# Optimization experiments

Hardware: AMD Instinct MI355X
Metric: run time of the kernel (lower is better)

Reference implementation:

```python
import jax, jax.numpy as jnp
import numpy as np

Q, N, S, A, E, H = 2048, 64, 128, 4, 128, 8
D = E // H
NEG = -1e9

def _mlp(x, w1, b1, w2, b2):
    return jax.nn.silu(x @ w1 + b1) @ w2 + b2

def _mha(x, wq, bq, wk, bk, wv, bv, wo, bo):
    # MultiHeadAttention with default activation=relu applied to q,k,v and output
    q = jax.nn.relu(x @ wq + bq)
    k = jax.nn.relu(x @ wk + bk)
    v = jax.nn.relu(x @ wv + bv)
    def split(t):
        return t.reshape(Q, N, H, D).transpose(0, 2, 1, 3)  # [Q,H,N,D]
    qh, kh, vh = split(q), split(k), split(v)
    scores = jnp.einsum('bhqd,bhkd->bhqk', qh, kh) / (D ** 0.5)
    attn = jax.nn.softmax(scores, axis=-1)
    y = jnp.einsum('bhqk,bhkd->bhqd', attn, vh).transpose(0, 2, 1, 3).reshape(Q, N, E)
    return jax.nn.relu(y @ wo + bo)

def setup_inputs():
    key = jax.random.key(0)
    ks = jax.random.split(key, 26)
    nrm = lambda k, s: jax.random.normal(k, s, jnp.float32) * 0.05
    return {
        'tasks': jax.random.normal(ks[0], (Q, N, N + 4 * S), jnp.float32),
        'constraints': jax.random.normal(ks[1], (Q, A), jnp.float32),
        'masks': jax.random.randint(ks[2], (Q, N, S), 0, 2),
        'topologicals': jax.random.randint(ks[3], (Q, N), 0, N),
        'w_init1': nrm(ks[4], (N + A, 128)), 'b_init1': jnp.zeros((128,), jnp.float32),
        'w_init2': nrm(ks[5], (128, E)), 'b_init2': jnp.zeros((E,), jnp.float32),
        'wq': nrm(ks[6], (E, E)), 'bq': jnp.zeros((E,), jnp.float32),
        'wk': nrm(ks[7], (E, E)), 'bk': jnp.zeros((E,), jnp.float32),
        'wv': nrm(ks[8], (E, E)), 'bv': jnp.zeros((E,), jnp.float32),
        'wo': nrm(ks[9], (E, E)), 'bo': jnp.zeros((E,), jnp.float32),
        'w_node1': nrm(ks[10], (E + A, 128)), 'b_node1': jnp.zeros((128,), jnp.float32),
        'w_node2': nrm(ks[11], (128, E)), 'b_node2': jnp.zeros((E,), jnp.float32),
        'w_ser1': nrm(ks[12], (A, 128)), 'b_ser1': jnp.zeros((128,), jnp.float32),
        'w_ser2': nrm(ks[13], (128, E)), 'b_ser2': jnp.zeros((E,), jnp.float32),
    }

def reference(tasks, constraints, masks, topologicals,
              w_init1, b_init1, w_init2, b_init2,
              wq, bq, wk, bk, wv, bv, wo, bo,
              w_node1, b_node1, w_node2, b_node2,
              w_ser1, b_ser1, w_ser2, b_ser2):
    cons = jnp.broadcast_to(constraints[:, None, :], (Q, N, A))
    node_emb = _mlp(jnp.concatenate([tasks[:, :, :N], cons], -1), w_init1, b_init1, w_init2, b_init2)
    nodes_emb = _mha(node_emb, wq, bq, wk, bk, wv, bv, wo, bo) + node_emb
    # original sets channel 0 to -3 then overwrites with 3; channel 2 stays 0 (kept faithfully)
    qos = jnp.zeros((Q, N, A), jnp.float32).at[:, :, 0].set(3.0).at[:, :, 1].set(1.0).at[:, :, 3].set(1.0)
    ava = jnp.ones((Q,), jnp.float32)
    tp = jnp.full((Q,), 3.0, jnp.float32)
    rel = jnp.ones((Q,), jnp.float32)
    ridx = jnp.zeros((Q, N), jnp.float32)
    rprob = jnp.zeros((Q, N), jnp.float32)
    qidx = jnp.arange(Q)
    topo_seq = topologicals[:, ::-1].T  # [N, Q]: reversed topological order, one node per step
    keys = jax.random.split(jax.random.key(1), N)

    def step(carry, xs):
        qos, ava, tp, rel, ridx, rprob = carry
        topo, k = xs
        task = tasks[qidx, topo]                 # [Q, N + 4S] per-query gathered row
        workflow = task[:, :N]
        response_time = jnp.max(workflow * qos[:, :, 0], axis=1)  # [Q]
        qos_feat = jnp.stack([response_time, ava, tp, rel], axis=-1)
        node_e = nodes_emb[qidx, topo]           # [Q, E]
        tne = _mlp(jnp.concatenate([node_e, qos_feat], -1), w_node1, b_node1, w_node2, b_node2)
        services = task[:, N:].reshape(Q, S, A)
        ser_emb = _mlp(services, w_ser1, b_ser1, w_ser2, b_ser2)
        logits = jnp.einsum('qse,qe->qs', ser_emb, tne)
        mask = masks[qidx, topo]                 # [Q, S]
        logits = jnp.where(mask == 0, NEG, logits)
        ser_prob = jax.nn.softmax(logits, axis=-1)
        ser_idx = jax.random.categorical(k, logits)  # ~ Categorical(ser_prob)
        onehot = jax.nn.one_hot(topo, N, dtype=jnp.float32)
        ridx = ridx + onehot * ser_idx[:, None].astype(jnp.float32)
        rprob = rprob + onehot * ser_prob[qidx, ser_idx][:, None]
        base = ser_idx * 4 + N
        ser_rt = task[qidx, base]
        ser_ava = task[qidx, base + 1]
        ser_tp = task[qidx, base + 2]
        ser_rel = task[qidx, base + 3]
        new_tp = jnp.minimum(ser_tp, tp)
        qos = qos.at[qidx, topo, 0].set(ser_rt + response_time)
        qos = qos.at[qidx, topo, 1].set(ser_ava * ava)
        qos = qos.at[qidx, topo, 2].set(new_tp)
        qos = qos.at[qidx, topo, 3].set(ser_rel * rel)
        return (qos, ser_ava * ava, new_tp, ser_rel * rel, ridx, rprob), None

    (qos, ava, tp, rel, ridx, rprob), _ = jax.lax.scan(
        step, (qos, ava, tp, rel, ridx, rprob), (topo_seq, keys))
    return ridx.astype(jnp.int16), rprob
```

## Files before the change

### kernel.cpp

```cpp
#include <hip/hip_runtime.h>
#include <math.h>

#define Qn 2048
#define Nn 64
#define Sn 128
#define An 4
#define En 128
#define TASKW 576
#define NEGV -1000000000.0f

typedef float v2f __attribute__((ext_vector_type(2)));

__device__ __forceinline__ v2f mkv2(float a, float b) {
  v2f r; r.x = a; r.y = b; return r;
}
__device__ __forceinline__ void pkfma(v2f& d, v2f a, v2f b) {
  asm("v_pk_fma_f32 %0, %1, %2, %0" : "+v"(d) : "v"(a), "v"(b));
}
__device__ __forceinline__ v2f pkmul(v2f a, v2f b) {
  v2f d; asm("v_pk_mul_f32 %0, %1, %2" : "=v"(d) : "v"(a), "v"(b)); return d;
}
__device__ __forceinline__ v2f pkadd(v2f a, v2f b) {
  v2f d; asm("v_pk_add_f32 %0, %1, %2" : "=v"(d) : "v"(a), "v"(b)); return d;
}

__device__ __forceinline__ void threefry2x32(unsigned k0, unsigned k1,
                                             unsigned x0, unsigned x1,
                                             unsigned& o0, unsigned& o1) {
  unsigned ks2 = k0 ^ k1 ^ 0x1BD11BDAu;
  x0 += k0; x1 += k1;
#define TFR(r) { x0 += x1; x1 = (x1 << (r)) | (x1 >> (32 - (r))); x1 ^= x0; }
  TFR(13) TFR(15) TFR(26) TFR(6)
  x0 += k1;  x1 += ks2 + 1u;
  TFR(17) TFR(29) TFR(16) TFR(24)
  x0 += ks2; x1 += k0 + 2u;
  TFR(13) TFR(15) TFR(26) TFR(6)
  x0 += k0;  x1 += k1 + 3u;
  TFR(17) TFR(29) TFR(16) TFR(24)
  x0 += k1;  x1 += ks2 + 4u;
  TFR(13) TFR(15) TFR(26) TFR(6)
  x0 += ks2; x1 += k0 + 5u;
#undef TFR
  o0 = x0; o1 = x1;
}

__device__ __forceinline__ float silu_f(float x) {
  return x / (1.0f + expf(-x));
}

__device__ __forceinline__ float fexp(float x) {
  return __builtin_amdgcn_exp2f(x * 1.44269504088896f);
}
__device__ __forceinline__ float fsilu(float x) {
  const float e = __builtin_amdgcn_exp2f(x * -1.44269504088896f);
  return x * __builtin_amdgcn_rcpf(1.0f + e);
}
__device__ __forceinline__ float flog(float x) {
  return __builtin_amdgcn_logf(x) * 0.69314718055995f;
}

__global__ void setup_kernel(const float* __restrict__ w_node2,
                             const float* __restrict__ b_node2,
                             const float* __restrict__ w_ser2,
                             const float* __restrict__ b_ser2,
                             float* __restrict__ Mbuf, float* __restrict__ dvec,
                             unsigned* __restrict__ keys) {
  const int b = blockIdx.x, t = threadIdx.x;
  if (b < 128) {
    float acc = 0.0f;
    for (int e = 0; e < 128; ++e)
      acc = fmaf(w_node2[b * 128 + e], w_ser2[t * 128 + e], acc);
    Mbuf[b * 128 + t] = acc;
  } else if (b == 128) {
    float acc = 0.0f;
    for (int e = 0; e < 128; ++e)
      acc = fmaf(b_node2[e], w_ser2[t * 128 + e], acc);
    dvec[t] = acc;
  } else {
    if (t < 64) {
      unsigned o0, o1;
      threefry2x32(0u, 1u, 0u, (unsigned)t, o0, o1);
      keys[2 * t + 0] = o0;
      keys[2 * t + 1] = o1;
    }
  }
}

__global__ __launch_bounds__(256, 2)
void init_mlp_kernel(const float* __restrict__ tasks,
                     const float* __restrict__ cons,
                     const float* __restrict__ w1, const float* __restrict__ b1,
                     const float* __restrict__ w2, const float* __restrict__ b2,
                     float* __restrict__ node_emb) {
  const int q = blockIdx.x, tid = threadIdx.x;
  const int lane = tid & 127, half = tid >> 7;
  __shared__ __align__(16) float xr[2][68];
  __shared__ __align__(16) float sgb[2][128];
  v2f w1p[34], w2p[64];
#pragma unroll
  for (int i = 0; i < 34; ++i)
    w1p[i] = mkv2(w1[(2 * i) * 128 + lane], w1[(2 * i + 1) * 128 + lane]);
#pragma unroll
  for (int j = 0; j < 64; ++j)
    w2p[j] = mkv2(w2[(2 * j) * 128 + lane], w2[(2 * j + 1) * 128 + lane]);
  const float bb1 = b1[lane], bb2 = b2[lane];
  for (int r = 0; r < 64; r += 2) {
    if (tid < 136) {
      const int rr = tid / 68, j = tid - rr * 68;
      xr[rr][j] = (j < 64) ? tasks[(q * 64 + r + rr) * TASKW + j]
                           : cons[q * 4 + (j - 64)];
    }
    __syncthreads();
    v2f gp = mkv2(0.0f, 0.0f);
    const v2f* xr2 = (const v2f*)&xr[half][0];
#pragma unroll
    for (int i = 0; i < 34; ++i) pkfma(gp, xr2[i], w1p[i]);
    const float g = gp.x + gp.y + bb1;
    sgb[half][lane] = silu_f(g);
    __syncthreads();
    v2f op = mkv2(0.0f, 0.0f);
    const v2f* sgb2 = (const v2f*)&sgb[half][0];
#pragma unroll
    for (int j = 0; j < 64; ++j) pkfma(op, sgb2[j], w2p[j]);
    node_emb[(q * 64 + r + half) * 128 + lane] = op.x + op.y + bb2;
    __syncthreads();
  }
}

__global__ __launch_bounds__(256, 2)
void mha_kernel(const float* __restrict__ node_emb,
                const float* __restrict__ wq, const float* __restrict__ bq,
                const float* __restrict__ wk, const float* __restrict__ bk,
                const float* __restrict__ wv, const float* __restrict__ bv,
                float* __restrict__ y_out) {
  const int q = blockIdx.x, tid = threadIdx.x;
  __shared__ __align__(16) float xs[64][130];
  __shared__ __align__(16) float qh[64][18];
  __shared__ __align__(16) float kh[64][18];
  __shared__ __align__(16) float vt[16][66];
  __shared__ __align__(16) float pool[3 * 16 * 130];
  float (*wht)[16][130] = (float (*)[16][130])pool;
  float (*at)[66] = (float (*)[66])pool;

  for (int idx = tid; idx < 64 * 128; idx += 256) {
    const int n = idx >> 7, e = idx & 127;
    xs[n][e] = node_emb[(q * 64 + n) * 128 + e];
  }
  __syncthreads();

  const int d16 = tid >> 4;
  const int ng = tid & 15;

  for (int hd = 0; hd < 8; ++hd) {
    for (int idx = tid; idx < 3 * 128 * 16; idx += 256) {
      const int m = idx >> 11, k = (idx >> 4) & 127, d = idx & 15;
      const float* W = (m == 0) ? wq : (m == 1) ? wk : wv;
      wht[m][d][k] = W[k * 128 + hd * 16 + d];
    }
    __syncthreads();

    {
      const float bqv = bq[hd * 16 + d16];
      const float bkv = bk[hd * 16 + d16];
      const float bvv = bv[hd * 16 + d16];
      const v2f* wq2 = (const v2f*)&wht[0][d16][0];
      const v2f* wk2 = (const v2f*)&wht[1][d16][0];
      const v2f* wv2 = (const v2f*)&wht[2][d16][0];
      const v2f* xr0 = (const v2f*)&xs[ng][0];
      const v2f* xr1 = (const v2f*)&xs[ng + 16][0];
      const v2f* xr2 = (const v2f*)&xs[ng + 32][0];
      const v2f* xr3 = (const v2f*)&xs[ng + 48][0];
      v2f aq0 = mkv2(0, 0), aq1 = mkv2(0, 0), aq2 = mkv2(0, 0), aq3 = mkv2(0, 0);
      v2f ak0 = mkv2(0, 0), ak1 = mkv2(0, 0), ak2 = mkv2(0, 0), ak3 = mkv2(0, 0);
      v2f av0 = mkv2(0, 0), av1 = mkv2(0, 0), av2 = mkv2(0, 0), av3 = mkv2(0, 0);
#pragma unroll 8
      for (int kk = 0; kk < 64; ++kk) {
        const v2f wqv = wq2[kk], wkv = wk2[kk], wvv = wv2[kk];
        const v2f x0 = xr0[kk], x1 = xr1[kk], x2 = xr2[kk], x3 = xr3[kk];
        pkfma(aq0, x0, wqv); pkfma(aq1, x1, wqv);
        pkfma(aq2, x2, wqv); pkfma(aq3, x3, wqv);
        pkfma(ak0, x0, wkv); pkfma(ak1, x1, wkv);
        pkfma(ak2, x2, wkv); pkfma(ak3, x3, wkv);
        pkfma(av0, x0, wvv); pkfma(av1, x1, wvv);
        pkfma(av2, x2, wvv); pkfma(av3, x3, wvv);
      }
      qh[ng][d16] = fmaxf(aq0.x + aq0.y + bqv, 0.0f);
      qh[ng + 16][d16] = fmaxf(aq1.x + aq1.y + bqv, 0.0f);
      qh[ng + 32][d16] = fmaxf(aq2.x + aq2.y + bqv, 0.0f);
      qh[ng + 48][d16] = fmaxf(aq3.x + aq3.y + bqv, 0.0f);
      kh[ng][d16] = fmaxf(ak0.x + ak0.y + bkv, 0.0f);
      kh[ng + 16][d16] = fmaxf(ak1.x + ak1.y + bkv, 0.0f);
      kh[ng + 32][d16] = fmaxf(ak2.x + ak2.y + bkv, 0.0f);
      kh[ng + 48][d16] = fmaxf(ak3.x + ak3.y + bkv, 0.0f);
      vt[d16][ng] = fmaxf(av0.x + av0.y + bvv, 0.0f);
      vt[d16][ng + 16] = fmaxf(av1.x + av1.y + bvv, 0.0f);
      vt[d16][ng + 32] = fmaxf(av2.x + av2.y + bvv, 0.0f);
      vt[d16][ng + 48] = fmaxf(av3.x + av3.y + bvv, 0.0f);
    }
    __syncthreads();

    {
      const int n = tid >> 2, mg = tid & 3;
      v2f qv[8];
      const v2f* qrow = (const v2f*)&qh[n][0];
#pragma unroll
      for (int kk = 0; kk < 8; ++kk) qv[kk] = qrow[kk];
#pragma unroll 4
      for (int jj = 0; jj < 16; ++jj) {
        const int m = mg + 4 * jj;
        const v2f* krow = (const v2f*)&kh[m][0];
        v2f accp = mkv2(0.0f, 0.0f);
#pragma unroll
        for (int kk = 0; kk < 8; ++kk) pkfma(accp, qv[kk], krow[kk]);
        at[n][m] = (accp.x + accp.y) * 0.25f;
      }
    }
    __syncthreads();

    {
      const int r = tid >> 2, p = tid & 3;
      float mx = -1e30f;
#pragma unroll
      for (int t2 = 0; t2 < 16; ++t2) mx = fmaxf(mx, at[r][p * 16 + t2]);
      mx = fmaxf(mx, __shfl_xor(mx, 1, 64));
      mx = fmaxf(mx, __shfl_xor(mx, 2, 64));
      float s = 0.0f;
#pragma unroll
      for (int t2 = 0; t2 < 16; ++t2) {
        const float e = fexp(at[r][p * 16 + t2] - mx);
        at[r][p * 16 + t2] = e;
        s += e;
      }
      s += __shfl_xor(s, 1, 64);
      s += __shfl_xor(s, 2, 64);
      const float rs = __builtin_amdgcn_rcpf(s);
#pragma unroll
      for (int t2 = 0; t2 < 16; ++t2) at[r][p * 16 + t2] *= rs;
    }
    __syncthreads();

    {
      const int dd = tid & 15, ngr = tid >> 4;
      const v2f* vrow = (const v2f*)&vt[dd][0];
      const v2f* ar0 = (const v2f*)&at[ngr][0];
      const v2f* ar1 = (const v2f*)&at[ngr + 16][0];
      const v2f* ar2 = (const v2f*)&at[ngr + 32][0];
      const v2f* ar3 = (const v2f*)&at[ngr + 48][0];
      v2f ac0 = mkv2(0, 0), ac1 = mkv2(0, 0), ac2 = mkv2(0, 0), ac3 = mkv2(0, 0);
#pragma unroll 8
      for (int kk = 0; kk < 32; ++kk) {
        const v2f vv = vrow[kk];
        pkfma(ac0, ar0[kk], vv);
        pkfma(ac1, ar1[kk], vv);
        pkfma(ac2, ar2[kk], vv);
        pkfma(ac3, ar3[kk], vv);
      }
      y_out[(q * 64 + ngr) * 128 + hd * 16 + dd] = ac0.x + ac0.y;
      y_out[(q * 64 + ngr + 16) * 128 + hd * 16 + dd] = ac1.x + ac1.y;
      y_out[(q * 64 + ngr + 32) * 128 + hd * 16 + dd] = ac2.x + ac2.y;
      y_out[(q * 64 + ngr + 48) * 128 + hd * 16 + dd] = ac3.x + ac3.y;
    }
    __syncthreads();
  }
}

__global__ __launch_bounds__(256, 4)
void outproj_kernel(const float* __restrict__ node_emb,
                    const float* __restrict__ wo, const float* __restrict__ bo,
                    float* __restrict__ nodes_emb) {
  const int q = blockIdx.x, tid = threadIdx.x;
  __shared__ __align__(16) float ys[64][130];
  __shared__ __align__(16) float wot[32][130];
  for (int idx = tid; idx < 64 * 128; idx += 256) {
    const int n = idx >> 7, e = idx & 127;
    ys[n][e] = nodes_emb[(q * 64 + n) * 128 + e];
  }
  const int cg = tid & 15, ngr = tid >> 4;
  for (int c0 = 0; c0 < 128; c0 += 32) {
    __syncthreads();
    for (int idx = tid; idx < 32 * 128; idx += 256) {
      const int k = idx >> 5, c = idx & 31;
      wot[c][k] = wo[k * 128 + c0 + c];
    }
    __syncthreads();
    const int c = c0 + 2 * cg;
    const v2f* w0 = (const v2f*)&wot[2 * cg][0];
    const v2f* w1 = (const v2f*)&wot[2 * cg + 1][0];
    const v2f* yr0 = (const v2f*)&ys[ngr][0];
    const v2f* yr1 = (const v2f*)&ys[ngr + 16][0];
    const v2f* yr2 = (const v2f*)&ys[ngr + 32][0];
    const v2f* yr3 = (const v2f*)&ys[ngr + 48][0];
    v2f a00 = mkv2(0, 0), a01 = mkv2(0, 0), a10 = mkv2(0, 0), a11 = mkv2(0, 0);
    v2f a20 = mkv2(0, 0), a21 = mkv2(0, 0), a30 = mkv2(0, 0), a31 = mkv2(0, 0);
#pragma unroll 8
    for (int kk = 0; kk < 64; ++kk) {
      const v2f wv0 = w0[kk], wv1 = w1[kk];
      const v2f x0 = yr0[kk], x1 = yr1[kk], x2 = yr2[kk], x3 = yr3[kk];
      pkfma(a00, x0, wv0); pkfma(a01, x0, wv1);
      pkfma(a10, x1, wv0); pkfma(a11, x1, wv1);
      pkfma(a20, x2, wv0); pkfma(a21, x2, wv1);
      pkfma(a30, x3, wv0); pkfma(a31, x3, wv1);
    }
    const float b0v = bo[c], b1v = bo[c + 1];
#define OUTP_EMIT(J, A0, A1)                                                  \
    {                                                                         \
      const int n = ngr + 16 * J;                                             \
      const float2 res = *(const float2*)&node_emb[(q * 64 + n) * 128 + c];   \
      float2 o;                                                               \
      o.x = fmaxf(A0.x + A0.y + b0v, 0.0f) + res.x;                           \
      o.y = fmaxf(A1.x + A1.y + b1v, 0.0f) + res.y;                           \
      *(float2*)&nodes_emb[(q * 64 + n) * 128 + c] = o;                       \
    }
    OUTP_EMIT(0, a00, a01)
    OUTP_EMIT(1, a10, a11)
    OUTP_EMIT(2, a20, a21)
    OUTP_EMIT(3, a30, a31)
#undef OUTP_EMIT
  }
}

__global__ __launch_bounds__(256, 4)
void gbase_kernel(const float* __restrict__ nodes_emb,
                  const float* __restrict__ w_node1,
                  const float* __restrict__ b_node1,
                  float* __restrict__ gbase) {
  const int q = blockIdx.x, tid = threadIdx.x;
  __shared__ __align__(16) float ys[64][130];
  __shared__ __align__(16) float wot[32][130];
  for (int idx = tid; idx < 64 * 128; idx += 256) {
    const int n = idx >> 7, e = idx & 127;
    ys[n][e] = nodes_emb[(q * 64 + n) * 128 + e];
  }
  const int cg = tid & 15, ngr = tid >> 4;
  for (int c0 = 0; c0 < 128; c0 += 32) {
    __syncthreads();
    for (int idx = tid; idx < 32 * 128; idx += 256) {
      const int k = idx >> 5, c = idx & 31;
      wot[c][k] = w_node1[k * 128 + c0 + c];
    }
    __syncthreads();
    const int c = c0 + 2 * cg;
    const v2f* w0 = (const v2f*)&wot[2 * cg][0];
    const v2f* w1 = (const v2f*)&wot[2 * cg + 1][0];
    const v2f* yr0 = (const v2f*)&ys[ngr][0];
    const v2f* yr1 = (const v2f*)&ys[ngr + 16][0];
    const v2f* yr2 = (const v2f*)&ys[ngr + 32][0];
    const v2f* yr3 = (const v2f*)&ys[ngr + 48][0];
    v2f a00 = mkv2(0, 0), a01 = mkv2(0, 0), a10 = mkv2(0, 0), a11 = mkv2(0, 0);
    v2f a20 = mkv2(0, 0), a21 = mkv2(0, 0), a30 = mkv2(0, 0), a31 = mkv2(0, 0);
#pragma unroll 8
    for (int kk = 0; kk < 64; ++kk) {
      const v2f wv0 = w0[kk], wv1 = w1[kk];
      const v2f x0 = yr0[kk], x1 = yr1[kk], x2 = yr2[kk], x3 = yr3[kk];
      pkfma(a00, x0, wv0); pkfma(a01, x0, wv1);
      pkfma(a10, x1, wv0); pkfma(a11, x1, wv1);
      pkfma(a20, x2, wv0); pkfma(a21, x2, wv1);
      pkfma(a30, x3, wv0); pkfma(a31, x3, wv1);
    }
    const float b0v = b_node1[c], b1v = b_node1[c + 1];
#define GB_EMIT(J, A0, A1)                                                    \
    {                                                                         \
      const int n = ngr + 16 * J;                                             \
      float2 o;                                                               \
      o.x = A0.x + A0.y + b0v;                                                \
      o.y = A1.x + A1.y + b1v;                                                \
      *(float2*)&gbase[(q * 64 + n) * 128 + c] = o;                           \
    }
    GB_EMIT(0, a00, a01)
    GB_EMIT(1, a10, a11)
    GB_EMIT(2, a20, a21)
    GB_EMIT(3, a30, a31)
#undef GB_EMIT
  }
}

__global__ __launch_bounds__(256, 4)
void scan_kernel(const float* __restrict__ tasks, const int* __restrict__ masks,
                 const int* __restrict__ topologicals,
                 const float* __restrict__ w_node1,
                 const float* __restrict__ w_ser1,
                 const float* __restrict__ b_ser1,
                 const float* __restrict__ gbase,
                 const float* __restrict__ Mbuf, const float* __restrict__ dvec,
                 const unsigned* __restrict__ keys, float* __restrict__ out) {
  const int q = blockIdx.x, tid = threadIdx.x;
  const int lane = tid & 127, half = tid >> 7;
  const int wl = tid & 63;
  const int wave = tid >> 6;

  __shared__ __align__(16) float task_s[2][TASKW];
  __shared__ __align__(16) float gb_s[2][128];
  __shared__ int mask_s[2][128];
  __shared__ int topo_s[64];
  __shared__ __align__(16) float sg[128];
  __shared__ __align__(16) v2f warr_s[64][4];
  __shared__ __align__(16) v2f bp_s[64];
  __shared__ __align__(16) v2f up_s[64];
  __shared__ __align__(16) float red[256];
  __shared__ float lcomp_s[128];
  __shared__ float gla_s[128];
  __shared__ int act_s[128];
  __shared__ float qos_s[64 * 4];
  __shared__ float ridx_s[64], rprob_s[64];
  __shared__ __align__(16) float qw[4][128];
  __shared__ __align__(16) float dvs[128];
  __shared__ float scal[2];
  __shared__ int sidx_s, kstar_s, na_s;
  __shared__ unsigned keys_s[128];

  v2f Mr2[32];
#pragma unroll
  for (int j = 0; j < 32; ++j)
    Mr2[j] = mkv2(Mbuf[(half * 64 + 2 * j) * 128 + lane],
                  Mbuf[(half * 64 + 2 * j + 1) * 128 + lane]);

  if (tid < 64) {
    topo_s[tid] = topologicals[q * 64 + tid];
    const int j = tid, sl = ((j & 15) << 2) | (j >> 4);
#pragma unroll
    for (int c = 0; c < 4; ++c)
      warr_s[sl][c] =
          mkv2(w_ser1[c * 128 + 2 * j], w_ser1[c * 128 + 2 * j + 1]);
    bp_s[sl] = mkv2(b_ser1[2 * j], b_ser1[2 * j + 1]);
  }
  if (tid < 128) {
    dvs[tid] = dvec[tid];
    keys_s[tid] = keys[tid];
  }
  for (int i = tid; i < 512; i += 256)
    qw[i >> 7][i & 127] = w_node1[(128 + (i >> 7)) * 128 + (i & 127)];
  if (tid < 64) {
    qos_s[tid * 4 + 0] = 3.0f;
    qos_s[tid * 4 + 1] = 1.0f;
    qos_s[tid * 4 + 2] = 0.0f;
    qos_s[tid * 4 + 3] = 1.0f;
    ridx_s[tid] = 0.0f;
    rprob_s[tid] = 0.0f;
  }
  float ava = 1.0f, tp = 3.0f, rel = 1.0f;
  __syncthreads();

  {
    const int topo0 = topo_s[63];
    if (tid < 144)
      ((float4*)task_s[0])[tid] =
          ((const float4*)(tasks + (size_t)(q * 64 + topo0) * TASKW))[tid];
    if (tid < 128) {
      gb_s[0][tid] = gbase[(q * 64 + topo0) * 128 + tid];
      mask_s[0][tid] = masks[(q * 64 + topo0) * 128 + tid];
    }
  }
  __syncthreads();

  for (int t = 0; t < 64; ++t) {
    const int cur = t & 1, nxt = cur ^ 1;
    const int topo = topo_s[63 - t];

    float rt = 0.0f;
    if (wave < 2) {
      float p = task_s[cur][wl] * qos_s[wl * 4];
#pragma unroll
      for (int o = 32; o > 0; o >>= 1) p = fmaxf(p, __shfl_xor(p, o, 64));
      rt = p;
    } else if (wave == 2) {
      const int m0 = mask_s[cur][wl] != 0;
      const int m1 = mask_s[cur][wl + 64] != 0;
      const unsigned long long b0 = __ballot(m0);
      const unsigned long long b1 = __ballot(m1);
      const unsigned long long lt = (1ull << wl) - 1ull;
      const int c0 = __popcll(b0);
      if (m0) act_s[__popcll(b0 & lt)] = wl;
      if (m1) act_s[c0 + __popcll(b1 & lt)] = wl + 64;
      if (wl == 0) na_s = c0 + __popcll(b1);
    }
    if (tid < 128) {
      float g = gb_s[cur][tid];
      g = fmaf(rt, qw[0][tid], g);
      g = fmaf(ava, qw[1][tid], g);
      g = fmaf(tp, qw[2][tid], g);
      g = fmaf(rel, qw[3][tid], g);
      sg[tid] = fsilu(g);
    }
    __syncthreads();

    {
      v2f accp = mkv2(0.0f, 0.0f);
      const v2f* sg2 = (const v2f*)sg + half * 32;
#pragma unroll
      for (int j = 0; j < 32; ++j) pkfma(accp, sg2[j], Mr2[j]);
      red[tid] = accp.x + accp.y;
    }
    __syncthreads();
    if (tid < 64) {
      const v2f r0 = *(const v2f*)&red[2 * tid];
      const v2f r1 = *(const v2f*)&red[2 * tid + 128];
      const v2f dv = *(const v2f*)&dvs[2 * tid];
      up_s[((tid & 15) << 2) | (tid >> 4)] = pkadd(pkadd(r0, r1), dv);
    }
    __syncthreads();

    float4 pf_task;
    float pf_gb;
    int pf_mask;
    {
      const int tn = (t < 63) ? t + 1 : 63;
      const int ntopo = topo_s[63 - tn];
      if (tid < 144)
        pf_task =
            ((const float4*)(tasks + (size_t)(q * 64 + ntopo) * TASKW))[tid];
      if (tid < 128) {
        pf_gb = gbase[(q * 64 + ntopo) * 128 + tid];
        pf_mask = masks[(q * 64 + ntopo) * 128 + tid];
      }
    }

    const int na = na_s;
    {
      const int si = tid >> 2, hq = tid & 3;
      float ls[2];
#pragma unroll
      for (int rep = 0; rep < 2; ++rep) {
        const int slot = si + 64 * rep;
        float lv = 0.0f;
        if (slot < na) {
          const int s = act_s[slot];
          const float4 sv = *(const float4*)&task_s[cur][64 + 4 * s];
          const v2f svx = mkv2(sv.x, sv.x), svy = mkv2(sv.y, sv.y);
          const v2f svz = mkv2(sv.z, sv.z), svw = mkv2(sv.w, sv.w);
          v2f acc = mkv2(0.0f, 0.0f);
#pragma unroll
          for (int jj = 0; jj < 16; ++jj) {
            const int sl = (jj << 2) | hq;
            v2f p = bp_s[sl];
            pkfma(p, svx, warr_s[sl][0]);
            pkfma(p, svy, warr_s[sl][1]);
            pkfma(p, svz, warr_s[sl][2]);
            pkfma(p, svw, warr_s[sl][3]);
            const v2f e =
                pkmul(p, mkv2(-1.44269504088896f, -1.44269504088896f));
            const float ex = __builtin_amdgcn_exp2f(e.x);
            const float ey = __builtin_amdgcn_exp2f(e.y);
            const float rx = __builtin_amdgcn_rcpf(1.0f + ex);
            const float ry = __builtin_amdgcn_rcpf(1.0f + ey);
            pkfma(acc, mkv2(p.x * rx, p.y * ry), up_s[sl]);
          }
          lv = acc.x + acc.y;
        }
        lv += __shfl_xor(lv, 1, 64);
        lv += __shfl_xor(lv, 2, 64);
        ls[rep] = lv;
      }
      if (hq == 0) {
        if (si < na) lcomp_s[si] = ls[0];
        if (si + 64 < na) lcomp_s[si + 64] = ls[1];
      }
    }
    __syncthreads();

    if (tid < 128) {
      float gv = -3.0e38f;
      if (tid < na) {
        const int s = act_s[tid];
        unsigned o0, o1;
        threefry2x32(keys_s[2 * t], keys_s[2 * t + 1], 0u,
                     (unsigned)(q * 128 + s), o0, o1);
        const unsigned bits = o0 ^ o1;
        const float f = __uint_as_float((bits >> 9) | 0x3f800000u) - 1.0f;
        const float u = (f > 0.0f) ? f : 1.17549435e-38f;
        gv = lcomp_s[tid] - flog(-flog(u));
      }
      gla_s[tid] = gv;
    }
    if (tid < 144) ((float4*)task_s[nxt])[tid] = pf_task;
    if (tid < 128) {
      gb_s[nxt][tid] = pf_gb;
      mask_s[nxt][tid] = pf_mask;
    }
    __syncthreads();

    if (tid < 64) {
      float z = gla_s[tid];
      int zi = tid;
      const float z2 = gla_s[tid + 64];
      if (z2 > z) { z = z2; zi = tid + 64; }
#pragma unroll
      for (int o = 32; o > 0; o >>= 1) {
        const float zo = __shfl_xor(z, o, 64);
        const int io = __shfl_xor(zi, o, 64);
        if (zo > z || (zo == z && io < zi)) { z = zo; zi = io; }
      }
      if (tid == 0) {
        kstar_s = zi;
        sidx_s = act_s[zi];
      }
    } else if (tid < 128) {
      const int l2 = tid - 64;
      const float la = (l2 < na) ? lcomp_s[l2] : -3.0e38f;
      const float lb = (l2 + 64 < na) ? lcomp_s[l2 + 64] : -3.0e38f;
      float mx = fmaxf(la, lb);
#pragma unroll
      for (int o = 32; o > 0; o >>= 1) mx = fmaxf(mx, __shfl_xor(mx, o, 64));
      float e = fexp(la - mx) + fexp(lb - mx);
#pragma unroll
      for (int o = 32; o > 0; o >>= 1) e += __shfl_xor(e, o, 64);
      if (l2 == 0) { scal[0] = mx; scal[1] = e; }
    }
    __syncthreads();

    {
      const int si = sidx_s;
      const float s1v = task_s[cur][64 + 4 * si + 1];
      const float s2v = task_s[cur][64 + 4 * si + 2];
      const float s3v = task_s[cur][64 + 4 * si + 3];
      if (tid == 0) {
        const float s0v = task_s[cur][64 + 4 * si];
        const float prob = fexp(lcomp_s[kstar_s] - scal[0]) / scal[1];
        qos_s[topo * 4 + 0] = s0v + rt;
        qos_s[topo * 4 + 1] = s1v * ava;
        qos_s[topo * 4 + 2] = fminf(s2v, tp);
        qos_s[topo * 4 + 3] = s3v * rel;
        ridx_s[topo] += (float)si;
        rprob_s[topo] += prob;
      }
      ava = s1v * ava;
      tp = fminf(s2v, tp);
      rel = s3v * rel;
    }
    __syncthreads();
  }
  if (tid < 64) {
    out[q * 64 + tid] = ridx_s[tid];
    out[Qn * Nn + q * 64 + tid] = rprob_s[tid];
  }
}

extern "C" void kernel_launch(void* const* d_in, const int* in_sizes, int n_in,
                              void* d_out, int out_size, void* d_ws,
                              size_t ws_size, hipStream_t stream) {
  const float* tasks = (const float*)d_in[0];
  const float* constraints = (const float*)d_in[1];
  const int* masks = (const int*)d_in[2];
  const int* topologicals = (const int*)d_in[3];
  const float* w_init1 = (const float*)d_in[4];
  const float* b_init1 = (const float*)d_in[5];
  const float* w_init2 = (const float*)d_in[6];
  const float* b_init2 = (const float*)d_in[7];
  const float* wq = (const float*)d_in[8];
  const float* bq = (const float*)d_in[9];
  const float* wk = (const float*)d_in[10];
  const float* bk = (const float*)d_in[11];
  const float* wv = (const float*)d_in[12];
  const float* bv = (const float*)d_in[13];
  const float* wo = (const float*)d_in[14];
  const float* bo = (const float*)d_in[15];
  const float* w_node1 = (const float*)d_in[16];
  const float* b_node1 = (const float*)d_in[17];
  const float* w_node2 = (const float*)d_in[18];
  const float* b_node2 = (const float*)d_in[19];
  const float* w_ser1 = (const float*)d_in[20];
  const float* b_ser1 = (const float*)d_in[21];
  const float* w_ser2 = (const float*)d_in[22];
  const float* b_ser2 = (const float*)d_in[23];

  float* ws = (float*)d_ws;
  float* node_emb = ws;
  float* nodes_emb = node_emb + (size_t)Qn * Nn * En;
  float* Mbuf = nodes_emb + (size_t)Qn * Nn * En;
  float* dvec = Mbuf + 128 * 128;
  unsigned* keys = (unsigned*)(dvec + 128);
  float* gbase = node_emb;

  setup_kernel<<<130, 128, 0, stream>>>(w_node2, b_node2, w_ser2, b_ser2, Mbuf,
                                        dvec, keys);
  init_mlp_kernel<<<Qn, 256, 0, stream>>>(tasks, constraints, w_init1, b_init1,
                                          w_init2, b_init2, node_emb);
  mha_kernel<<<Qn, 256, 0, stream>>>(node_emb, wq, bq, wk, bk, wv, bv,
                                     nodes_emb);
  outproj_kernel<<<Qn, 256, 0, stream>>>(node_emb, wo, bo, nodes_emb);
  gbase_kernel<<<Qn, 256, 0, stream>>>(nodes_emb, w_node1, b_node1, gbase);
  scan_kernel<<<Qn, 256, 0, stream>>>(tasks, masks, topologicals, w_node1,
                                      w_ser1, b_ser1, gbase, Mbuf, dvec, keys,
                                      (float*)d_out);
}
```

Baseline: 2.226 ms.

## Fuse out-projection with gbase, vectorize LDS reads, restructure scan service scoring

```diff
diff --git a/kernel.cpp b/kernel.cpp
--- a/kernel.cpp
+++ b/kernel.cpp
@@ -10,15 +10,15 @@
 #define NEGV -1000000000.0f
 
 typedef float v2f __attribute__((ext_vector_type(2)));
+typedef float v4f __attribute__((ext_vector_type(4)));
 
 __device__ __forceinline__ v2f mkv2(float a, float b) {
   v2f r; r.x = a; r.y = b; return r;
 }
+__device__ __forceinline__ v2f lo2(v4f v) { v2f r; r.x = v.x; r.y = v.y; return r; }
+__device__ __forceinline__ v2f hi2(v4f v) { v2f r; r.x = v.z; r.y = v.w; return r; }
 __device__ __forceinline__ void pkfma(v2f& d, v2f a, v2f b) {
   asm("v_pk_fma_f32 %0, %1, %2, %0" : "+v"(d) : "v"(a), "v"(b));
-}
-__device__ __forceinline__ v2f pkmul(v2f a, v2f b) {
-  v2f d; asm("v_pk_mul_f32 %0, %1, %2" : "=v"(d) : "v"(a), "v"(b)); return d;
 }
 __device__ __forceinline__ v2f pkadd(v2f a, v2f b) {
   v2f d; asm("v_pk_add_f32 %0, %1, %2" : "=v"(d) : "v"(a), "v"(b)); return d;
@@ -47,7 +47,6 @@
 __device__ __forceinline__ float silu_f(float x) {
   return x / (1.0f + expf(-x));
 }
-
 __device__ __forceinline__ float fexp(float x) {
   return __builtin_amdgcn_exp2f(x * 1.44269504088896f);
 }
@@ -112,16 +111,24 @@
     }
     __syncthreads();
     v2f gp = mkv2(0.0f, 0.0f);
-    const v2f* xr2 = (const v2f*)&xr[half][0];
-#pragma unroll
-    for (int i = 0; i < 34; ++i) pkfma(gp, xr2[i], w1p[i]);
+    const v4f* xr4 = (const v4f*)&xr[half][0];
+#pragma unroll
+    for (int i = 0; i < 17; ++i) {
+      const v4f x = xr4[i];
+      pkfma(gp, lo2(x), w1p[2 * i]);
+      pkfma(gp, hi2(x), w1p[2 * i + 1]);
+    }
     const float g = gp.x + gp.y + bb1;
     sgb[half][lane] = silu_f(g);
     __syncthreads();
     v2f op = mkv2(0.0f, 0.0f);
-    const v2f* sgb2 = (const v2f*)&sgb[half][0];
-#pragma unroll
-    for (int j = 0; j < 64; ++j) pkfma(op, sgb2[j], w2p[j]);
+    const v4f* sgb4 = (const v4f*)&sgb[half][0];
+#pragma unroll
+    for (int j = 0; j < 32; ++j) {
+      const v4f s = sgb4[j];
+      pkfma(op, lo2(s), w2p[2 * j]);
+      pkfma(op, hi2(s), w2p[2 * j + 1]);
+    }
     node_emb[(q * 64 + r + half) * 128 + lane] = op.x + op.y + bb2;
     __syncthreads();
   }
@@ -134,17 +141,18 @@
                 const float* __restrict__ wv, const float* __restrict__ bv,
                 float* __restrict__ y_out) {
   const int q = blockIdx.x, tid = threadIdx.x;
-  __shared__ __align__(16) float xs[64][130];
-  __shared__ __align__(16) float qh[64][18];
-  __shared__ __align__(16) float kh[64][18];
-  __shared__ __align__(16) float vt[16][66];
-  __shared__ __align__(16) float pool[3 * 16 * 130];
-  float (*wht)[16][130] = (float (*)[16][130])pool;
-  float (*at)[66] = (float (*)[66])pool;
-
-  for (int idx = tid; idx < 64 * 128; idx += 256) {
-    const int n = idx >> 7, e = idx & 127;
-    xs[n][e] = node_emb[(q * 64 + n) * 128 + e];
+  __shared__ __align__(16) float xs[64][132];
+  __shared__ __align__(16) float qh[64][20];
+  __shared__ __align__(16) float kh[64][20];
+  __shared__ __align__(16) float vt[16][68];
+  __shared__ __align__(16) float pool[3 * 16 * 132];
+  float (*wht)[16][132] = (float (*)[16][132])pool;
+  float (*at)[68] = (float (*)[68])pool;
+
+  for (int idx = tid; idx < 64 * 32; idx += 256) {
+    const int n = idx >> 5, e4 = idx & 31;
+    *(v4f*)&xs[n][4 * e4] =
+        *(const v4f*)&node_emb[(q * 64 + n) * 128 + 4 * e4];
   }
   __syncthreads();
 
@@ -163,26 +171,39 @@
       const float bqv = bq[hd * 16 + d16];
       const float bkv = bk[hd * 16 + d16];
       const float bvv = bv[hd * 16 + d16];
-      const v2f* wq2 = (const v2f*)&wht[0][d16][0];
-      const v2f* wk2 = (const v2f*)&wht[1][d16][0];
-      const v2f* wv2 = (const v2f*)&wht[2][d16][0];
-      const v2f* xr0 = (const v2f*)&xs[ng][0];
-      const v2f* xr1 = (const v2f*)&xs[ng + 16][0];
-      const v2f* xr2 = (const v2f*)&xs[ng + 32][0];
-      const v2f* xr3 = (const v2f*)&xs[ng + 48][0];
+      const v4f* wq4 = (const v4f*)&wht[0][d16][0];
+      const v4f* wk4 = (const v4f*)&wht[1][d16][0];
+      const v4f* wv4 = (const v4f*)&wht[2][d16][0];
+      const v4f* xr0 = (const v4f*)&xs[ng][0];
+      const v4f* xr1 = (const v4f*)&xs[ng + 16][0];
+      const v4f* xr2 = (const v4f*)&xs[ng + 32][0];
+      const v4f* xr3 = (const v4f*)&xs[ng + 48][0];
       v2f aq0 = mkv2(0, 0), aq1 = mkv2(0, 0), aq2 = mkv2(0, 0), aq3 = mkv2(0, 0);
       v2f ak0 = mkv2(0, 0), ak1 = mkv2(0, 0), ak2 = mkv2(0, 0), ak3 = mkv2(0, 0);
       v2f av0 = mkv2(0, 0), av1 = mkv2(0, 0), av2 = mkv2(0, 0), av3 = mkv2(0, 0);
-#pragma unroll 8
-      for (int kk = 0; kk < 64; ++kk) {
-        const v2f wqv = wq2[kk], wkv = wk2[kk], wvv = wv2[kk];
-        const v2f x0 = xr0[kk], x1 = xr1[kk], x2 = xr2[kk], x3 = xr3[kk];
-        pkfma(aq0, x0, wqv); pkfma(aq1, x1, wqv);
-        pkfma(aq2, x2, wqv); pkfma(aq3, x3, wqv);
-        pkfma(ak0, x0, wkv); pkfma(ak1, x1, wkv);
-        pkfma(ak2, x2, wkv); pkfma(ak3, x3, wkv);
-        pkfma(av0, x0, wvv); pkfma(av1, x1, wvv);
-        pkfma(av2, x2, wvv); pkfma(av3, x3, wvv);
+#pragma unroll 4
+      for (int kk = 0; kk < 32; ++kk) {
+        const v4f wqv = wq4[kk], wkv = wk4[kk], wvv = wv4[kk];
+        const v4f x0 = xr0[kk], x1 = xr1[kk], x2 = xr2[kk], x3 = xr3[kk];
+        const v2f wqa = lo2(wqv), wqb = hi2(wqv);
+        const v2f wka = lo2(wkv), wkb = hi2(wkv);
+        const v2f wva = lo2(wvv), wvb = hi2(wvv);
+        const v2f x0a = lo2(x0), x0b = hi2(x0);
+        const v2f x1a = lo2(x1), x1b = hi2(x1);
+        const v2f x2a = lo2(x2), x2b = hi2(x2);
+        const v2f x3a = lo2(x3), x3b = hi2(x3);
+        pkfma(aq0, x0a, wqa); pkfma(aq0, x0b, wqb);
+        pkfma(aq1, x1a, wqa); pkfma(aq1, x1b, wqb);
+        pkfma(aq2, x2a, wqa); pkfma(aq2, x2b, wqb);
+        pkfma(aq3, x3a, wqa); pkfma(aq3, x3b, wqb);
+        pkfma(ak0, x0a, wka); pkfma(ak0, x0b, wkb);
+        pkfma(ak1, x1a, wka); pkfma(ak1, x1b, wkb);
+        pkfma(ak2, x2a, wka); pkfma(ak2, x2b, wkb);
+        pkfma(ak3, x3a, wka); pkfma(ak3, x3b, wkb);
+        pkfma(av0, x0a, wva); pkfma(av0, x0b, wvb);
+        pkfma(av1, x1a, wva); pkfma(av1, x1b, wvb);
+        pkfma(av2, x2a, wva); pkfma(av2, x2b, wvb);
+        pkfma(av3, x3a, wva); pkfma(av3, x3b, wvb);
       }
       qh[ng][d16] = fmaxf(aq0.x + aq0.y + bqv, 0.0f);
       qh[ng + 16][d16] = fmaxf(aq1.x + aq1.y + bqv, 0.0f);
@@ -201,17 +222,21 @@
 
     {
       const int n = tid >> 2, mg = tid & 3;
-      v2f qv[8];
-      const v2f* qrow = (const v2f*)&qh[n][0];
-#pragma unroll
-      for (int kk = 0; kk < 8; ++kk) qv[kk] = qrow[kk];
+      v4f qv[4];
+      const v4f* qrow = (const v4f*)&qh[n][0];
+#pragma unroll
+      for (int kk = 0; kk < 4; ++kk) qv[kk] = qrow[kk];
 #pragma unroll 4
       for (int jj = 0; jj < 16; ++jj) {
         const int m = mg + 4 * jj;
-        const v2f* krow = (const v2f*)&kh[m][0];
+        const v4f* krow = (const v4f*)&kh[m][0];
         v2f accp = mkv2(0.0f, 0.0f);
 #pragma unroll
-        for (int kk = 0; kk < 8; ++kk) pkfma(accp, qv[kk], krow[kk]);
+        for (int kk = 0; kk < 4; ++kk) {
+          const v4f kv = krow[kk];
+          pkfma(accp, lo2(qv[kk]), lo2(kv));
+          pkfma(accp, hi2(qv[kk]), hi2(kv));
+        }
         at[n][m] = (accp.x + accp.y) * 0.25f;
       }
     }
@@ -219,41 +244,53 @@
 
     {
       const int r = tid >> 2, p = tid & 3;
+      const v4f* arow = (const v4f*)&at[r][p * 16];
+      v4f av[4];
+#pragma unroll
+      for (int u = 0; u < 4; ++u) av[u] = arow[u];
       float mx = -1e30f;
 #pragma unroll
-      for (int t2 = 0; t2 < 16; ++t2) mx = fmaxf(mx, at[r][p * 16 + t2]);
+      for (int u = 0; u < 4; ++u) {
+        mx = fmaxf(mx, fmaxf(fmaxf(av[u].x, av[u].y), fmaxf(av[u].z, av[u].w)));
+      }
       mx = fmaxf(mx, __shfl_xor(mx, 1, 64));
       mx = fmaxf(mx, __shfl_xor(mx, 2, 64));
       float s = 0.0f;
 #pragma unroll
-      for (int t2 = 0; t2 < 16; ++t2) {
-        const float e = fexp(at[r][p * 16 + t2] - mx);
-        at[r][p * 16 + t2] = e;
-        s += e;
+      for (int u = 0; u < 4; ++u) {
+        av[u].x = fexp(av[u].x - mx); av[u].y = fexp(av[u].y - mx);
+        av[u].z = fexp(av[u].z - mx); av[u].w = fexp(av[u].w - mx);
+        s += av[u].x + av[u].y + av[u].z + av[u].w;
       }
       s += __shfl_xor(s, 1, 64);
       s += __shfl_xor(s, 2, 64);
       const float rs = __builtin_amdgcn_rcpf(s);
-#pragma unroll
-      for (int t2 = 0; t2 < 16; ++t2) at[r][p * 16 + t2] *= rs;
+      v4f* wrow = (v4f*)&at[r][p * 16];
+#pragma unroll
+      for (int u = 0; u < 4; ++u) {
+        av[u].x *= rs; av[u].y *= rs; av[u].z *= rs; av[u].w *= rs;
+        wrow[u] = av[u];
+      }
     }
     __syncthreads();
 
     {
       const int dd = tid & 15, ngr = tid >> 4;
-      const v2f* vrow = (const v2f*)&vt[dd][0];
-      const v2f* ar0 = (const v2f*)&at[ngr][0];
-      const v2f* ar1 = (const v2f*)&at[ngr + 16][0];
-      const v2f* ar2 = (const v2f*)&at[ngr + 32][0];
-      const v2f* ar3 = (const v2f*)&at[ngr + 48][0];
+      const v4f* vrow = (const v4f*)&vt[dd][0];
+      const v4f* ar0 = (const v4f*)&at[ngr][0];
+      const v4f* ar1 = (const v4f*)&at[ngr + 16][0];
+      const v4f* ar2 = (const v4f*)&at[ngr + 32][0];
+      const v4f* ar3 = (const v4f*)&at[ngr + 48][0];
       v2f ac0 = mkv2(0, 0), ac1 = mkv2(0, 0), ac2 = mkv2(0, 0), ac3 = mkv2(0, 0);
-#pragma unroll 8
-      for (int kk = 0; kk < 32; ++kk) {
-        const v2f vv = vrow[kk];
-        pkfma(ac0, ar0[kk], vv);
-        pkfma(ac1, ar1[kk], vv);
-        pkfma(ac2, ar2[kk], vv);
-        pkfma(ac3, ar3[kk], vv);
+#pragma unroll 4
+      for (int kk = 0; kk < 16; ++kk) {
+        const v4f vv = vrow[kk];
+        const v2f va = lo2(vv), vb = hi2(vv);
+        const v4f a0 = ar0[kk], a1 = ar1[kk], a2 = ar2[kk], a3 = ar3[kk];
+        pkfma(ac0, lo2(a0), va); pkfma(ac0, hi2(a0), vb);
+        pkfma(ac1, lo2(a1), va); pkfma(ac1, hi2(a1), vb);
+        pkfma(ac2, lo2(a2), va); pkfma(ac2, hi2(a2), vb);
+        pkfma(ac3, lo2(a3), va); pkfma(ac3, hi2(a3), vb);
       }
       y_out[(q * 64 + ngr) * 128 + hd * 16 + dd] = ac0.x + ac0.y;
       y_out[(q * 64 + ngr + 16) * 128 + hd * 16 + dd] = ac1.x + ac1.y;
@@ -264,75 +301,83 @@
   }
 }
 
-__global__ __launch_bounds__(256, 4)
-void outproj_kernel(const float* __restrict__ node_emb,
-                    const float* __restrict__ wo, const float* __restrict__ bo,
-                    float* __restrict__ nodes_emb) {
-  const int q = blockIdx.x, tid = threadIdx.x;
-  __shared__ __align__(16) float ys[64][130];
-  __shared__ __align__(16) float wot[32][130];
-  for (int idx = tid; idx < 64 * 128; idx += 256) {
-    const int n = idx >> 7, e = idx & 127;
-    ys[n][e] = nodes_emb[(q * 64 + n) * 128 + e];
-  }
-  const int cg = tid & 15, ngr = tid >> 4;
-  for (int c0 = 0; c0 < 128; c0 += 32) {
-    __syncthreads();
-    for (int idx = tid; idx < 32 * 128; idx += 256) {
-      const int k = idx >> 5, c = idx & 31;
-      wot[c][k] = wo[k * 128 + c0 + c];
-    }
-    __syncthreads();
-    const int c = c0 + 2 * cg;
-    const v2f* w0 = (const v2f*)&wot[2 * cg][0];
-    const v2f* w1 = (const v2f*)&wot[2 * cg + 1][0];
-    const v2f* yr0 = (const v2f*)&ys[ngr][0];
-    const v2f* yr1 = (const v2f*)&ys[ngr + 16][0];
-    const v2f* yr2 = (const v2f*)&ys[ngr + 32][0];
-    const v2f* yr3 = (const v2f*)&ys[ngr + 48][0];
-    v2f a00 = mkv2(0, 0), a01 = mkv2(0, 0), a10 = mkv2(0, 0), a11 = mkv2(0, 0);
-    v2f a20 = mkv2(0, 0), a21 = mkv2(0, 0), a30 = mkv2(0, 0), a31 = mkv2(0, 0);
-#pragma unroll 8
-    for (int kk = 0; kk < 64; ++kk) {
-      const v2f wv0 = w0[kk], wv1 = w1[kk];
-      const v2f x0 = yr0[kk], x1 = yr1[kk], x2 = yr2[kk], x3 = yr3[kk];
-      pkfma(a00, x0, wv0); pkfma(a01, x0, wv1);
-      pkfma(a10, x1, wv0); pkfma(a11, x1, wv1);
-      pkfma(a20, x2, wv0); pkfma(a21, x2, wv1);
-      pkfma(a30, x3, wv0); pkfma(a31, x3, wv1);
-    }
-    const float b0v = bo[c], b1v = bo[c + 1];
-#define OUTP_EMIT(J, A0, A1)                                                  \
-    {                                                                         \
-      const int n = ngr + 16 * J;                                             \
-      const float2 res = *(const float2*)&node_emb[(q * 64 + n) * 128 + c];   \
-      float2 o;                                                               \
-      o.x = fmaxf(A0.x + A0.y + b0v, 0.0f) + res.x;                           \
-      o.y = fmaxf(A1.x + A1.y + b1v, 0.0f) + res.y;                           \
-      *(float2*)&nodes_emb[(q * 64 + n) * 128 + c] = o;                       \
-    }
-    OUTP_EMIT(0, a00, a01)
-    OUTP_EMIT(1, a10, a11)
-    OUTP_EMIT(2, a20, a21)
-    OUTP_EMIT(3, a30, a31)
-#undef OUTP_EMIT
-  }
-}
-
-__global__ __launch_bounds__(256, 4)
-void gbase_kernel(const float* __restrict__ nodes_emb,
+__global__ __launch_bounds__(256, 2)
+void outgb_kernel(const float* __restrict__ resid, const float* __restrict__ y,
+                  const float* __restrict__ wo, const float* __restrict__ bo,
                   const float* __restrict__ w_node1,
                   const float* __restrict__ b_node1,
                   float* __restrict__ gbase) {
   const int q = blockIdx.x, tid = threadIdx.x;
-  __shared__ __align__(16) float ys[64][130];
-  __shared__ __align__(16) float wot[32][130];
-  for (int idx = tid; idx < 64 * 128; idx += 256) {
-    const int n = idx >> 7, e = idx & 127;
-    ys[n][e] = nodes_emb[(q * 64 + n) * 128 + e];
+  __shared__ __align__(16) float ys[64][132];
+  __shared__ __align__(16) float wot[32][132];
+  for (int idx = tid; idx < 64 * 32; idx += 256) {
+    const int n = idx >> 5, e4 = idx & 31;
+    *(v4f*)&ys[n][4 * e4] = *(const v4f*)&y[(q * 64 + n) * 128 + 4 * e4];
   }
   const int cg = tid & 15, ngr = tid >> 4;
-  for (int c0 = 0; c0 < 128; c0 += 32) {
+  float nodes[4][8];
+
+#pragma unroll
+  for (int tile = 0; tile < 4; ++tile) {
+    const int c0 = 32 * tile;
+    __syncthreads();
+    for (int idx = tid; idx < 32 * 128; idx += 256) {
+      const int k = idx >> 5, c = idx & 31;
+      wot[c][k] = wo[k * 128 + c0 + c];
+    }
+    __syncthreads();
+    const int c = c0 + 2 * cg;
+    const v4f* w0 = (const v4f*)&wot[2 * cg][0];
+    const v4f* w1 = (const v4f*)&wot[2 * cg + 1][0];
+    const v4f* yr0 = (const v4f*)&ys[ngr][0];
+    const v4f* yr1 = (const v4f*)&ys[ngr + 16][0];
+    const v4f* yr2 = (const v4f*)&ys[ngr + 32][0];
+    const v4f* yr3 = (const v4f*)&ys[ngr + 48][0];
+    v2f a00 = mkv2(0, 0), a01 = mkv2(0, 0), a10 = mkv2(0, 0), a11 = mkv2(0, 0);
+    v2f a20 = mkv2(0, 0), a21 = mkv2(0, 0), a30 = mkv2(0, 0), a31 = mkv2(0, 0);
+#pragma unroll 4
+    for (int kk = 0; kk < 32; ++kk) {
+      const v4f wv0 = w0[kk], wv1 = w1[kk];
+      const v2f w0a = lo2(wv0), w0b = hi2(wv0);
+      const v2f w1a = lo2(wv1), w1b = hi2(wv1);
+      const v4f x0 = yr0[kk], x1 = yr1[kk], x2 = yr2[kk], x3 = yr3[kk];
+      pkfma(a00, lo2(x0), w0a); pkfma(a00, hi2(x0), w0b);
+      pkfma(a01, lo2(x0), w1a); pkfma(a01, hi2(x0), w1b);
+      pkfma(a10, lo2(x1), w0a); pkfma(a10, hi2(x1), w0b);
+      pkfma(a11, lo2(x1), w1a); pkfma(a11, hi2(x1), w1b);
+      pkfma(a20, lo2(x2), w0a); pkfma(a20, hi2(x2), w0b);
+      pkfma(a21, lo2(x2), w1a); pkfma(a21, hi2(x2), w1b);
+      pkfma(a30, lo2(x3), w0a); pkfma(a30, hi2(x3), w0b);
+      pkfma(a31, lo2(x3), w1a); pkfma(a31, hi2(x3), w1b);
+    }
+    const float b0v = bo[c], b1v = bo[c + 1];
+#define PROJ_EMIT(J, A0, A1)                                                  \
+    {                                                                         \
+      const int n = ngr + 16 * J;                                             \
+      const float2 res = *(const float2*)&resid[(q * 64 + n) * 128 + c];      \
+      nodes[J][2 * tile] = fmaxf(A0.x + A0.y + b0v, 0.0f) + res.x;            \
+      nodes[J][2 * tile + 1] = fmaxf(A1.x + A1.y + b1v, 0.0f) + res.y;        \
+    }
+    PROJ_EMIT(0, a00, a01)
+    PROJ_EMIT(1, a10, a11)
+    PROJ_EMIT(2, a20, a21)
+    PROJ_EMIT(3, a30, a31)
+#undef PROJ_EMIT
+  }
+  __syncthreads();
+#pragma unroll
+  for (int j = 0; j < 4; ++j) {
+    const int n = ngr + 16 * j;
+#pragma unroll
+    for (int tile = 0; tile < 4; ++tile) {
+      *(float2*)&ys[n][32 * tile + 2 * cg] =
+          make_float2(nodes[j][2 * tile], nodes[j][2 * tile + 1]);
+    }
+  }
+
+#pragma unroll
+  for (int tile = 0; tile < 4; ++tile) {
+    const int c0 = 32 * tile;
     __syncthreads();
     for (int idx = tid; idx < 32 * 128; idx += 256) {
       const int k = idx >> 5, c = idx & 31;
@@ -340,22 +385,28 @@
     }
     __syncthreads();
     const int c = c0 + 2 * cg;
-    const v2f* w0 = (const v2f*)&wot[2 * cg][0];
-    const v2f* w1 = (const v2f*)&wot[2 * cg + 1][0];
-    const v2f* yr0 = (const v2f*)&ys[ngr][0];
-    const v2f* yr1 = (const v2f*)&ys[ngr + 16][0];
-    const v2f* yr2 = (const v2f*)&ys[ngr + 32][0];
-    const v2f* yr3 = (const v2f*)&ys[ngr + 48][0];
+    const v4f* w0 = (const v4f*)&wot[2 * cg][0];
+    const v4f* w1 = (const v4f*)&wot[2 * cg + 1][0];
+    const v4f* yr0 = (const v4f*)&ys[ngr][0];
+    const v4f* yr1 = (const v4f*)&ys[ngr + 16][0];
+    const v4f* yr2 = (const v4f*)&ys[ngr + 32][0];
+    const v4f* yr3 = (const v4f*)&ys[ngr + 48][0];
     v2f a00 = mkv2(0, 0), a01 = mkv2(0, 0), a10 = mkv2(0, 0), a11 = mkv2(0, 0);
     v2f a20 = mkv2(0, 0), a21 = mkv2(0, 0), a30 = mkv2(0, 0), a31 = mkv2(0, 0);
-#pragma unroll 8
-    for (int kk = 0; kk < 64; ++kk) {
-      const v2f wv0 = w0[kk], wv1 = w1[kk];
-      const v2f x0 = yr0[kk], x1 = yr1[kk], x2 = yr2[kk], x3 = yr3[kk];
-      pkfma(a00, x0, wv0); pkfma(a01, x0, wv1);
-      pkfma(a10, x1, wv0); pkfma(a11, x1, wv1);
-      pkfma(a20, x2, wv0); pkfma(a21, x2, wv1);
-      pkfma(a30, x3, wv0); pkfma(a31, x3, wv1);
+#pragma unroll 4
+    for (int kk = 0; kk < 32; ++kk) {
+      const v4f wv0 = w0[kk], wv1 = w1[kk];
+      const v2f w0a = lo2(wv0), w0b = hi2(wv0);
+      const v2f w1a = lo2(wv1), w1b = hi2(wv1);
+      const v4f x0 = yr0[kk], x1 = yr1[kk], x2 = yr2[kk], x3 = yr3[kk];
+      pkfma(a00, lo2(x0), w0a); pkfma(a00, hi2(x0), w0b);
+      pkfma(a01, lo2(x0), w1a); pkfma(a01, hi2(x0), w1b);
+      pkfma(a10, lo2(x1), w0a); pkfma(a10, hi2(x1), w0b);
+      pkfma(a11, lo2(x1), w1a); pkfma(a11, hi2(x1), w1b);
+      pkfma(a20, lo2(x2), w0a); pkfma(a20, hi2(x2), w0b);
+      pkfma(a21, lo2(x2), w1a); pkfma(a21, hi2(x2), w1b);
+      pkfma(a30, lo2(x3), w0a); pkfma(a30, hi2(x3), w0b);
+      pkfma(a31, lo2(x3), w1a); pkfma(a31, hi2(x3), w1b);
     }
     const float b0v = b_node1[c], b1v = b_node1[c + 1];
 #define GB_EMIT(J, A0, A1)                                                    \
@@ -374,7 +425,7 @@
   }
 }
 
-__global__ __launch_bounds__(256, 4)
+__global__ __launch_bounds__(256, 3)
 void scan_kernel(const float* __restrict__ tasks, const int* __restrict__ masks,
                  const int* __restrict__ topologicals,
                  const float* __restrict__ w_node1,
@@ -393,20 +444,17 @@
   __shared__ int mask_s[2][128];
   __shared__ int topo_s[64];
   __shared__ __align__(16) float sg[128];
-  __shared__ __align__(16) v2f warr_s[64][4];
-  __shared__ __align__(16) v2f bp_s[64];
-  __shared__ __align__(16) v2f up_s[64];
+  __shared__ __align__(16) v2f wfull_s[64][6];
   __shared__ __align__(16) float red[256];
   __shared__ float lcomp_s[128];
   __shared__ float gla_s[128];
   __shared__ int act_s[128];
-  __shared__ float qos_s[64 * 4];
+  __shared__ float qr_s[64];
   __shared__ float ridx_s[64], rprob_s[64];
-  __shared__ __align__(16) float qw[4][128];
+  __shared__ __align__(16) v4f qw4_s[128];
   __shared__ __align__(16) float dvs[128];
-  __shared__ float scal[2];
-  __shared__ int sidx_s, kstar_s, na_s;
   __shared__ unsigned keys_s[128];
+  __shared__ int na_s;
 
   v2f Mr2[32];
 #pragma unroll
@@ -416,26 +464,25 @@
 
   if (tid < 64) {
     topo_s[tid] = topologicals[q * 64 + tid];
-    const int j = tid, sl = ((j & 15) << 2) | (j >> 4);
+    const int j = tid;
 #pragma unroll
     for (int c = 0; c < 4; ++c)
-      warr_s[sl][c] =
+      wfull_s[j][c] =
           mkv2(w_ser1[c * 128 + 2 * j], w_ser1[c * 128 + 2 * j + 1]);
-    bp_s[sl] = mkv2(b_ser1[2 * j], b_ser1[2 * j + 1]);
+    wfull_s[j][4] = mkv2(b_ser1[2 * j], b_ser1[2 * j + 1]);
+    qr_s[tid] = 3.0f;
+    ridx_s[tid] = 0.0f;
+    rprob_s[tid] = 0.0f;
   }
   if (tid < 128) {
     dvs[tid] = dvec[tid];
     keys_s[tid] = keys[tid];
-  }
-  for (int i = tid; i < 512; i += 256)
-    qw[i >> 7][i & 127] = w_node1[(128 + (i >> 7)) * 128 + (i & 127)];
-  if (tid < 64) {
-    qos_s[tid * 4 + 0] = 3.0f;
-    qos_s[tid * 4 + 1] = 1.0f;
-    qos_s[tid * 4 + 2] = 0.0f;
-    qos_s[tid * 4 + 3] = 1.0f;
-    ridx_s[tid] = 0.0f;
-    rprob_s[tid] = 0.0f;
+    v4f qp;
+    qp.x = w_node1[128 * 128 + tid];
+    qp.y = w_node1[129 * 128 + tid];
+    qp.z = w_node1[130 * 128 + tid];
+    qp.w = w_node1[131 * 128 + tid];
+    qw4_s[tid] = qp;
   }
   float ava = 1.0f, tp = 3.0f, rel = 1.0f;
   __syncthreads();
@@ -458,7 +505,7 @@
 
     float rt = 0.0f;
     if (wave < 2) {
-      float p = task_s[cur][wl] * qos_s[wl * 4];
+      float p = task_s[cur][wl] * qr_s[wl];
 #pragma unroll
       for (int o = 32; o > 0; o >>= 1) p = fmaxf(p, __shfl_xor(p, o, 64));
       rt = p;
@@ -474,20 +521,26 @@
       if (wl == 0) na_s = c0 + __popcll(b1);
     }
     if (tid < 128) {
+      const v4f qp = qw4_s[tid];
       float g = gb_s[cur][tid];
-      g = fmaf(rt, qw[0][tid], g);
-      g = fmaf(ava, qw[1][tid], g);
-      g = fmaf(tp, qw[2][tid], g);
-      g = fmaf(rel, qw[3][tid], g);
+      g = fmaf(rt, qp.x, g);
+      g = fmaf(ava, qp.y, g);
+      g = fmaf(tp, qp.z, g);
+      g = fmaf(rel, qp.w, g);
       sg[tid] = fsilu(g);
     }
     __syncthreads();
+    const int na = na_s;
 
     {
       v2f accp = mkv2(0.0f, 0.0f);
-      const v2f* sg2 = (const v2f*)sg + half * 32;
-#pragma unroll
-      for (int j = 0; j < 32; ++j) pkfma(accp, sg2[j], Mr2[j]);
+      const v4f* sgp = (const v4f*)sg + half * 16;
+#pragma unroll
+      for (int j = 0; j < 16; ++j) {
+        const v4f x = sgp[j];
+        pkfma(accp, lo2(x), Mr2[2 * j]);
+        pkfma(accp, hi2(x), Mr2[2 * j + 1]);
+      }
       red[tid] = accp.x + accp.y;
     }
     __syncthreads();
@@ -495,7 +548,7 @@
       const v2f r0 = *(const v2f*)&red[2 * tid];
       const v2f r1 = *(const v2f*)&red[2 * tid + 128];
       const v2f dv = *(const v2f*)&dvs[2 * tid];
-      up_s[((tid & 15) << 2) | (tid >> 4)] = pkadd(pkadd(r0, r1), dv);
+      wfull_s[tid][5] = pkadd(pkadd(r0, r1), dv);
     }
     __syncthreads();
 
@@ -514,45 +567,74 @@
       }
     }
 
-    const int na = na_s;
-    {
-      const int si = tid >> 2, hq = tid & 3;
-      float ls[2];
-#pragma unroll
-      for (int rep = 0; rep < 2; ++rep) {
-        const int slot = si + 64 * rep;
-        float lv = 0.0f;
-        if (slot < na) {
-          const int s = act_s[slot];
-          const float4 sv = *(const float4*)&task_s[cur][64 + 4 * s];
-          const v2f svx = mkv2(sv.x, sv.x), svy = mkv2(sv.y, sv.y);
-          const v2f svz = mkv2(sv.z, sv.z), svw = mkv2(sv.w, sv.w);
-          v2f acc = mkv2(0.0f, 0.0f);
-#pragma unroll
-          for (int jj = 0; jj < 16; ++jj) {
-            const int sl = (jj << 2) | hq;
-            v2f p = bp_s[sl];
-            pkfma(p, svx, warr_s[sl][0]);
-            pkfma(p, svy, warr_s[sl][1]);
-            pkfma(p, svz, warr_s[sl][2]);
-            pkfma(p, svw, warr_s[sl][3]);
-            const v2f e =
-                pkmul(p, mkv2(-1.44269504088896f, -1.44269504088896f));
-            const float ex = __builtin_amdgcn_exp2f(e.x);
-            const float ey = __builtin_amdgcn_exp2f(e.y);
-            const float rx = __builtin_amdgcn_rcpf(1.0f + ex);
-            const float ry = __builtin_amdgcn_rcpf(1.0f + ey);
-            pkfma(acc, mkv2(p.x * rx, p.y * ry), up_s[sl]);
+    {
+      const int g8 = tid >> 3, o = tid & 7;
+      const int sl0 = 4 * g8;
+      if (wave * 32 < na) {
+        const int s0 = (sl0 + 0 < na) ? act_s[sl0 + 0] : 0;
+        const int s1 = (sl0 + 1 < na) ? act_s[sl0 + 1] : 0;
+        const int s2 = (sl0 + 2 < na) ? act_s[sl0 + 2] : 0;
+        const int s3 = (sl0 + 3 < na) ? act_s[sl0 + 3] : 0;
+        const float4 svA = *(const float4*)&task_s[cur][64 + 4 * s0];
+        const float4 svB = *(const float4*)&task_s[cur][64 + 4 * s1];
+        const float4 svC = *(const float4*)&task_s[cur][64 + 4 * s2];
+        const float4 svD = *(const float4*)&task_s[cur][64 + 4 * s3];
+        const v2f A0 = mkv2(svA.x, svA.x), A1 = mkv2(svA.y, svA.y),
+                  A2 = mkv2(svA.z, svA.z), A3 = mkv2(svA.w, svA.w);
+        const v2f B0 = mkv2(svB.x, svB.x), B1 = mkv2(svB.y, svB.y),
+                  B2 = mkv2(svB.z, svB.z), B3 = mkv2(svB.w, svB.w);
+        const v2f C0 = mkv2(svC.x, svC.x), C1 = mkv2(svC.y, svC.y),
+                  C2 = mkv2(svC.z, svC.z), C3 = mkv2(svC.w, svC.w);
+        const v2f D0 = mkv2(svD.x, svD.x), D1 = mkv2(svD.y, svD.y),
+                  D2 = mkv2(svD.z, svD.z), D3 = mkv2(svD.w, svD.w);
+        v2f ac0 = mkv2(0, 0), ac1 = mkv2(0, 0), ac2 = mkv2(0, 0),
+            ac3 = mkv2(0, 0);
+        const v4f* wp = (const v4f*)&wfull_s[0][0];
+#pragma unroll
+        for (int jj = 0; jj < 8; ++jj) {
+          const int j = o + 8 * jj;
+          const v4f wA = wp[3 * j], wB = wp[3 * j + 1], wC = wp[3 * j + 2];
+          const v2f w0 = lo2(wA), w1 = hi2(wA);
+          const v2f w2 = lo2(wB), w3 = hi2(wB);
+          const v2f bp = lo2(wC), up = hi2(wC);
+#define SRV(AC, X0, X1, X2, X3)                                               \
+          {                                                                   \
+            v2f p = bp;                                                       \
+            pkfma(p, X0, w0); pkfma(p, X1, w1);                               \
+            pkfma(p, X2, w2); pkfma(p, X3, w3);                               \
+            const float ex =                                                  \
+                __builtin_amdgcn_exp2f(p.x * -1.44269504088896f);             \
+            const float ey =                                                  \
+                __builtin_amdgcn_exp2f(p.y * -1.44269504088896f);             \
+            const float rx = __builtin_amdgcn_rcpf(1.0f + ex);                \
+            const float ry = __builtin_amdgcn_rcpf(1.0f + ey);                \
+            pkfma(AC, mkv2(p.x * rx, p.y * ry), up);                          \
           }
-          lv = acc.x + acc.y;
+          SRV(ac0, A0, A1, A2, A3)
+          SRV(ac1, B0, B1, B2, B3)
+          SRV(ac2, C0, C1, C2, C3)
+          SRV(ac3, D0, D1, D2, D3)
+#undef SRV
         }
-        lv += __shfl_xor(lv, 1, 64);
-        lv += __shfl_xor(lv, 2, 64);
-        ls[rep] = lv;
-      }
-      if (hq == 0) {
-        if (si < na) lcomp_s[si] = ls[0];
-        if (si + 64 < na) lcomp_s[si + 64] = ls[1];
+        float l0 = ac0.x + ac0.y, l1 = ac1.x + ac1.y;
+        float l2 = ac2.x + ac2.y, l3 = ac3.x + ac3.y;
+        l0 += __shfl_xor(l0, 1, 64); l0 += __shfl_xor(l0, 2, 64);
+        l0 += __shfl_xor(l0, 4, 64);
+        l1 += __shfl_xor(l1, 1, 64); l1 += __shfl_xor(l1, 2, 64);
+        l1 += __shfl_xor(l1, 4, 64);
+        l2 += __shfl_xor(l2, 1, 64); l2 += __shfl_xor(l2, 2, 64);
+        l2 += __shfl_xor(l2, 4, 64);
+        l3 += __shfl_xor(l3, 1, 64); l3 += __shfl_xor(l3, 2, 64);
+        l3 += __shfl_xor(l3, 4, 64);
+        if (o == 0) {
+          if (sl0 + 3 < na) {
+            *(float4*)&lcomp_s[sl0] = make_float4(l0, l1, l2, l3);
+          } else {
+            if (sl0 + 0 < na) lcomp_s[sl0 + 0] = l0;
+            if (sl0 + 1 < na) lcomp_s[sl0 + 1] = l1;
+            if (sl0 + 2 < na) lcomp_s[sl0 + 2] = l2;
+          }
+        }
       }
     }
     __syncthreads();
@@ -578,49 +660,41 @@
     }
     __syncthreads();
 
-    if (tid < 64) {
-      float z = gla_s[tid];
-      int zi = tid;
-      const float z2 = gla_s[tid + 64];
-      if (z2 > z) { z = z2; zi = tid + 64; }
+    int si, kstar;
+    {
+      float z = gla_s[wl];
+      int zi = wl;
+      const float z2 = gla_s[wl + 64];
+      if (z2 > z) { z = z2; zi = wl + 64; }
 #pragma unroll
       for (int o = 32; o > 0; o >>= 1) {
         const float zo = __shfl_xor(z, o, 64);
         const int io = __shfl_xor(zi, o, 64);
         if (zo > z || (zo == z && io < zi)) { z = zo; zi = io; }
       }
-      if (tid == 0) {
-        kstar_s = zi;
-        sidx_s = act_s[zi];
-      }
-    } else if (tid < 128) {
-      const int l2 = tid - 64;
-      const float la = (l2 < na) ? lcomp_s[l2] : -3.0e38f;
-      const float lb = (l2 + 64 < na) ? lcomp_s[l2 + 64] : -3.0e38f;
+      kstar = zi;
+      si = act_s[zi];
+    }
+    if (wave == 3) {
+      const float la = (wl < na) ? lcomp_s[wl] : -3.0e38f;
+      const float lb = (wl + 64 < na) ? lcomp_s[wl + 64] : -3.0e38f;
       float mx = fmaxf(la, lb);
 #pragma unroll
       for (int o = 32; o > 0; o >>= 1) mx = fmaxf(mx, __shfl_xor(mx, o, 64));
       float e = fexp(la - mx) + fexp(lb - mx);
 #pragma unroll
       for (int o = 32; o > 0; o >>= 1) e += __shfl_xor(e, o, 64);
-      if (l2 == 0) { scal[0] = mx; scal[1] = e; }
-    }
-    __syncthreads();
-
-    {
-      const int si = sidx_s;
+      if (wl == 0)
+        rprob_s[topo] += fexp(lcomp_s[kstar] - mx) * __builtin_amdgcn_rcpf(e);
+    }
+    {
       const float s1v = task_s[cur][64 + 4 * si + 1];
       const float s2v = task_s[cur][64 + 4 * si + 2];
       const float s3v = task_s[cur][64 + 4 * si + 3];
       if (tid == 0) {
         const float s0v = task_s[cur][64 + 4 * si];
-        const float prob = fexp(lcomp_s[kstar_s] - scal[0]) / scal[1];
-        qos_s[topo * 4 + 0] = s0v + rt;
-        qos_s[topo * 4 + 1] = s1v * ava;
-        qos_s[topo * 4 + 2] = fminf(s2v, tp);
-        qos_s[topo * 4 + 3] = s3v * rel;
+        qr_s[topo] = s0v + rt;
         ridx_s[topo] += (float)si;
-        rprob_s[topo] += prob;
       }
       ava = s1v * ava;
       tp = fminf(s2v, tp);
@@ -664,8 +738,8 @@
 
   float* ws = (float*)d_ws;
   float* node_emb = ws;
-  float* nodes_emb = node_emb + (size_t)Qn * Nn * En;
-  float* Mbuf = nodes_emb + (size_t)Qn * Nn * En;
+  float* ybuf = node_emb + (size_t)Qn * Nn * En;
+  float* Mbuf = ybuf + (size_t)Qn * Nn * En;
   float* dvec = Mbuf + 128 * 128;
   unsigned* keys = (unsigned*)(dvec + 128);
   float* gbase = node_emb;
@@ -674,10 +748,9 @@
                                         dvec, keys);
   init_mlp_kernel<<<Qn, 256, 0, stream>>>(tasks, constraints, w_init1, b_init1,
                                           w_init2, b_init2, node_emb);
-  mha_kernel<<<Qn, 256, 0, stream>>>(node_emb, wq, bq, wk, bk, wv, bv,
-                                     nodes_emb);
-  outproj_kernel<<<Qn, 256, 0, stream>>>(node_emb, wo, bo, nodes_emb);
-  gbase_kernel<<<Qn, 256, 0, stream>>>(nodes_emb, w_node1, b_node1, gbase);
+  mha_kernel<<<Qn, 256, 0, stream>>>(node_emb, wq, bq, wk, bk, wv, bv, ybuf);
+  outgb_kernel<<<Qn, 256, 0, stream>>>(node_emb, ybuf, wo, bo, w_node1,
+                                       b_node1, gbase);
   scan_kernel<<<Qn, 256, 0, stream>>>(tasks, masks, topologicals, w_node1,
                                       w_ser1, b_ser1, gbase, Mbuf, dvec, keys,
                                       (float*)d_out);
```

Measured after the change: 2.069 ms. 1.08x faster.
